# Optimization experiments

Hardware: AMD Instinct MI355X
Metric: run time of the kernel (lower is better)

Reference implementation:

```python
import jax, jax.numpy as jnp
import numpy as np
from jax import lax

B_, N_, DIM, HID, DST, NT, IR, DTR, HH, WW = 16, 4096, 192, 384, 16, 17, 128, 24, 64, 64


def _selective_scan(u, delta, A, Bs, Cs, D, delta_bias):
    # u, delta: (B, Din, L); A: (Din, N); Bs, Cs: (B, N, L); D, delta_bias: (Din,)
    delta = jax.nn.softplus(delta + delta_bias[None, :, None])
    dT = jnp.moveaxis(delta, 2, 0)   # (L, B, Din)
    uT = jnp.moveaxis(u, 2, 0)       # (L, B, Din)
    BT = jnp.moveaxis(Bs, 2, 0)      # (L, B, N)
    CT = jnp.moveaxis(Cs, 2, 0)      # (L, B, N)
    Bsz, Din, L = u.shape
    Nst = A.shape[1]
    h0 = jnp.zeros((Bsz, Din, Nst), u.dtype)

    def step(h, inp):
        d_l, u_l, b_l, c_l = inp
        da = jnp.exp(d_l[:, :, None] * A[None])              # (B, Din, N)
        h = da * h + (d_l * u_l)[:, :, None] * b_l[:, None, :]
        y = jnp.einsum('bdn,bn->bd', h, c_l)
        return h, y

    _, ys = lax.scan(step, h0, (dT, uT, BT, CT))
    y = jnp.moveaxis(ys, 0, 2)                               # (B, Din, L)
    return y + u * D[None, :, None]


def _assm_forward(x, token_weight, gumbel_noise, embB, route_w1, route_b1, route_w2,
                  route_b2, inproj_w, inproj_b, cpe_w, cpe_b, x_proj_w, dt_w, dt_b,
                  A_logs, Ds, norm_g, norm_b, outproj_w, outproj_b, H, W, gather_type):
    B, n, C = x.shape
    hidden = inproj_w.shape[0]
    dst = token_weight.shape[1]
    dtr = dt_w.shape[1]

    # routing + gumbel-softmax (hard, straight-through)
    full_emb = embB @ token_weight                           # (NT, d_state)
    hmid = jax.nn.gelu(x @ route_w1.T + route_b1)
    logits = jax.nn.log_softmax(hmid @ route_w2.T + route_b2, axis=-1)
    y_soft = jax.nn.softmax(logits + gumbel_noise, axis=-1)
    idx = jnp.argmax(y_soft, axis=-1)                        # (B, n)
    y_hard = jax.nn.one_hot(idx, logits.shape[-1], dtype=y_soft.dtype)
    cls_policy = y_hard + y_soft - lax.stop_gradient(y_soft)
    prompt = cls_policy @ full_emb                           # (B, n, d_state)

    det = lax.stop_gradient(idx)
    # (gather_type 3/5 keypoint-group remap omitted: gather_type == 1 here)
    sort_idx = jnp.argsort(det, axis=-1)                     # (B, n)
    inv_idx = jnp.argsort(sort_idx, axis=-1)                 # index_reverse

    # in_proj (1x1 conv == pointwise linear) then depthwise CPE gate
    xi = x @ inproj_w.T + inproj_b                           # (B, n, hidden)
    xg = xi.reshape(B, H, W, hidden).transpose(0, 3, 1, 2)   # NCHW
    cpe = lax.conv_general_dilated(xg, cpe_w, (1, 1), 'SAME',
                                   feature_group_count=hidden,
                                   dimension_numbers=('NCHW', 'OIHW', 'NCHW'))
    cpe = cpe + cpe_b[None, :, None, None]
    xg = xg * jax.nn.sigmoid(cpe)
    xflat = xg.reshape(B, hidden, n).transpose(0, 2, 1)      # (B, n, hidden)

    sem_x = jnp.take_along_axis(xflat, sort_idx[:, :, None], axis=1)

    # Selective_Scan core
    xs = sem_x.transpose(0, 2, 1)                            # (B, Din, L)
    x_dbl = jnp.einsum('bdl,cd->bcl', xs, x_proj_w)          # (B, dtr+2N, L)
    dts, Bs, Cs = jnp.split(x_dbl, [dtr, dtr + dst], axis=1)
    dts = jnp.einsum('brl,dr->bdl', dts, dt_w)
    if gather_type != 0:
        Cs = Cs + prompt.transpose(0, 2, 1)
    A = -jnp.exp(A_logs)
    y = _selective_scan(xs, dts, A, Bs, Cs, Ds, dt_b)        # (B, Din, L)
    y = y.transpose(0, 2, 1)                                 # (B, L, hidden)

    mu = jnp.mean(y, axis=-1, keepdims=True)
    var = jnp.mean(jnp.square(y - mu), axis=-1, keepdims=True)
    yn = (y - mu) / jnp.sqrt(var + 1e-5) * norm_g + norm_b
    out = yn @ outproj_w.T + outproj_b                       # (B, n, dim)
    out = jnp.take_along_axis(out, inv_idx[:, :, None], axis=1)
    return out


def setup_inputs() -> dict:
    key = jax.random.key(0)
    ks = jax.random.split(key, 16)

    def rn(k, sh, s=0.02):
        return jax.random.normal(k, sh, dtype=jnp.float32) * s

    u = jax.random.uniform(ks[0], (B_, N_, NT), jnp.float32, 1e-6, 1.0 - 1e-6)
    gumbel = -jnp.log(-jnp.log(u))

    # faithful dt bias init (inverse-softplus of log-uniform dt)
    rng = np.random.default_rng(0)
    dt = np.exp(rng.uniform(size=HID) * (np.log(0.1) - np.log(0.001)) + np.log(0.001))
    dt = np.clip(dt, 1e-4, None)
    inv_dt = dt + np.log(-np.expm1(-dt))

    A_logs = jnp.log(jnp.tile(jnp.arange(1, DST + 1, dtype=jnp.float32), (HID, 1)))

    return {
        'x': jax.random.normal(ks[1], (B_, N_, DIM), jnp.float32),
        'token_weight': rn(ks[2], (IR, DST), 0.1),
        'gumbel_noise': gumbel,
        'embB': jax.random.uniform(ks[3], (NT, IR), jnp.float32, -1.0 / NT, 1.0 / NT),
        'route_w1': rn(ks[4], (DIM // 3, DIM)),
        'route_b1': jnp.zeros((DIM // 3,), jnp.float32),
        'route_w2': rn(ks[5], (NT, DIM // 3)),
        'route_b2': jnp.zeros((NT,), jnp.float32),
        'inproj_w': rn(ks[6], (HID, DIM)),
        'inproj_b': jnp.zeros((HID,), jnp.float32),
        'cpe_w': rn(ks[7], (HID, 1, 3, 3), 0.1),
        'cpe_b': jnp.zeros((HID,), jnp.float32),
        'x_proj_w': rn(ks[8], (DTR + 2 * DST, HID)),
        'dt_w': jax.random.uniform(ks[9], (HID, DTR), jnp.float32, -DTR ** -0.5, DTR ** -0.5),
        'dt_b': jnp.asarray(inv_dt, jnp.float32),
        'A_logs': A_logs,
        'Ds': jnp.ones((HID,), jnp.float32),
        'norm_g': jnp.ones((HID,), jnp.float32),
        'norm_b': jnp.zeros((HID,), jnp.float32),
        'outproj_w': rn(ks[10], (DIM, HID)),
        'outproj_b': jnp.zeros((DIM,), jnp.float32),
        'H': HH,
        'W': WW,
        'gather_type': 1,
    }


def reference(x, token_weight, gumbel_noise, embB, route_w1, route_b1, route_w2,
              route_b2, inproj_w, inproj_b, cpe_w, cpe_b, x_proj_w, dt_w, dt_b,
              A_logs, Ds, norm_g, norm_b, outproj_w, outproj_b, H, W, gather_type):
    return _assm_forward(x, token_weight, gumbel_noise, embB, route_w1, route_b1,
                         route_w2, route_b2, inproj_w, inproj_b, cpe_w, cpe_b,
                         x_proj_w, dt_w, dt_b, A_logs, Ds, norm_g, norm_b,
                         outproj_w, outproj_b, H, W, gather_type)
```

## Files before the change

kernel.cpp:

```cpp
#include <hip/hip_runtime.h>
#include <math.h>

#define NB 16
#define NL 4096
#define ND 192
#define NH 384
#define NS 16
#define NTK 17
#define NIR 128
#define NR 24
#define NHH 64
#define NWW 64
#define NCHUNKS 64
#define CHUNKLEN 64
#define NTOK (NB*NL)

typedef __attribute__((ext_vector_type(8))) short short8;
typedef __attribute__((ext_vector_type(4))) float floatx4;

__device__ __forceinline__ float gelu_tanh(float x){
  return 0.5f*x*(1.0f + tanhf(0.7978845608028654f*(x + 0.044715f*x*x*x)));
}
__device__ __forceinline__ float softplus_f(float x){
  return (x > 20.0f) ? x : log1pf(expf(x));
}
__device__ __forceinline__ short f2bf(float f){
  unsigned u = __float_as_uint(f);
  unsigned r = (u + 0x7fffu + ((u >> 16) & 1u)) >> 16;
  return (short)r;
}

union Pack8 { uint4 v; short s[8]; };

__global__ void k_emb(const float* __restrict__ embB, const float* __restrict__ tw,
                      float* __restrict__ fe){
  for (int o = threadIdx.x; o < NTK*NS; o += 256){
    int t = o / NS, s = o % NS;
    float acc = 0.f;
    for (int i = 0; i < NIR; ++i) acc += embB[t*NIR+i]*tw[i*NS+s];
    fe[o] = acc;
  }
}

__global__ void k_cvtw(const float* __restrict__ inw, const float* __restrict__ ow,
                       const float* __restrict__ xpw, const float* __restrict__ dtw,
                       short* __restrict__ inwb, short* __restrict__ owb,
                       short* __restrict__ xpwb, short* __restrict__ dtwb){
  int i = blockIdx.x*256 + threadIdx.x;
  int stride = gridDim.x*256;
  for (int p = i; p < NH*ND; p += stride) inwb[p] = f2bf(inw[p]);
  for (int p = i; p < ND*NH; p += stride) owb[p] = f2bf(ow[p]);
  for (int p = i; p < 56*NH; p += stride) xpwb[p] = f2bf(xpw[p]);
  for (int p = i; p < NH*32; p += stride){
    int r = p >> 5, c = p & 31;
    dtwb[p] = (c < NR) ? f2bf(dtw[r*NR + c]) : (short)0;
  }
}

template<int EPI>
__global__ __launch_bounds__(256) void k_gemm(const float* __restrict__ A, int lda,
    const float* __restrict__ W, int ldw, const float* __restrict__ bias,
    float* __restrict__ C, int ldc, int N, int K){
  __shared__ float As[16][68];
  __shared__ float Ws[16][68];
  int tid = threadIdx.x;
  int m0 = blockIdx.x*64, n0 = blockIdx.y*64;
  int tx = tid & 15, ty = tid >> 4;
  int srow = tid >> 2, skseg = (tid & 3)*4;
  float acc[4][4] = {};
  for (int k0 = 0; k0 < K; k0 += 16){
    {
      const float* ap = A + (size_t)(m0+srow)*lda + k0 + skseg;
      float4 v = *(const float4*)ap;
      As[skseg+0][srow]=v.x; As[skseg+1][srow]=v.y;
      As[skseg+2][srow]=v.z; As[skseg+3][srow]=v.w;
    }
    {
      float4 v = {0.f,0.f,0.f,0.f};
      if (n0 + srow < N) v = *(const float4*)(W + (size_t)(n0+srow)*ldw + k0 + skseg);
      Ws[skseg+0][srow]=v.x; Ws[skseg+1][srow]=v.y;
      Ws[skseg+2][srow]=v.z; Ws[skseg+3][srow]=v.w;
    }
    __syncthreads();
    #pragma unroll
    for (int kk = 0; kk < 16; ++kk){
      float4 av = *(const float4*)&As[kk][ty*4];
      float4 wv = *(const float4*)&Ws[kk][tx*4];
      acc[0][0] += av.x*wv.x; acc[0][1] += av.x*wv.y;
      acc[0][2] += av.x*wv.z; acc[0][3] += av.x*wv.w;
      acc[1][0] += av.y*wv.x; acc[1][1] += av.y*wv.y;
      acc[1][2] += av.y*wv.z; acc[1][3] += av.y*wv.w;
      acc[2][0] += av.z*wv.x; acc[2][1] += av.z*wv.y;
      acc[2][2] += av.z*wv.z; acc[2][3] += av.z*wv.w;
      acc[3][0] += av.w*wv.x; acc[3][1] += av.w*wv.y;
      acc[3][2] += av.w*wv.z; acc[3][3] += av.w*wv.w;
    }
    __syncthreads();
  }
  #pragma unroll
  for (int i = 0; i < 4; ++i){
    int m = m0 + ty*4 + i;
    #pragma unroll
    for (int j = 0; j < 4; ++j){
      int n = n0 + tx*4 + j;
      if (n < N){
        float v = acc[i][j] + (bias ? bias[n] : 0.f);
        if (EPI==1) v = gelu_tanh(v);
        C[(size_t)m*ldc + n] = v;
      }
    }
  }
}

template<int EPI, int AF32, int LNA>
__global__ __launch_bounds__(256) void k_mfma(const void* __restrict__ Aptr, int lda,
    const short* __restrict__ Wbf, int ldw, const float* __restrict__ bias,
    float* __restrict__ C, int ldc, int N, int K, const int* __restrict__ remap,
    const float* __restrict__ lnm, const float* __restrict__ lnr,
    const float* __restrict__ lng, const float* __restrict__ lnb){
  __shared__ short As[128*40];
  __shared__ short Bs[64*40];
  int tid = threadIdx.x;
  int m0 = blockIdx.x*128, n0 = blockIdx.y*64;
  int w = tid >> 6, lane = tid & 63;
  int lq = lane >> 4, lr = lane & 15;
  floatx4 acc[2][4];
  #pragma unroll
  for (int i = 0; i < 2; ++i)
    #pragma unroll
    for (int j = 0; j < 4; ++j) acc[i][j] = (floatx4){0.f,0.f,0.f,0.f};
  int ar = tid >> 1, aq = (tid & 1)*2;
  int br = tid >> 2, bq = tid & 3;
  float mr = 0.f, rr = 0.f;
  if (LNA){ mr = lnm[m0+ar]; rr = lnr[m0+ar]; }
  for (int k0 = 0; k0 < K; k0 += 32){
    Pack8 sa0, sa1;
    if (AF32){
      const float* ap = (const float*)Aptr + (size_t)(m0+ar)*lda + k0 + aq*8;
      float f[16];
      float4 f0 = *(const float4*)(ap);
      float4 f1 = *(const float4*)(ap+4);
      float4 f2 = *(const float4*)(ap+8);
      float4 f3 = *(const float4*)(ap+12);
      f[0]=f0.x; f[1]=f0.y; f[2]=f0.z; f[3]=f0.w;
      f[4]=f1.x; f[5]=f1.y; f[6]=f1.z; f[7]=f1.w;
      f[8]=f2.x; f[9]=f2.y; f[10]=f2.z; f[11]=f2.w;
      f[12]=f3.x; f[13]=f3.y; f[14]=f3.z; f[15]=f3.w;
      if (LNA){
        const float* gp = lng + k0 + aq*8;
        const float* bp = lnb + k0 + aq*8;
        #pragma unroll
        for (int j = 0; j < 16; ++j) f[j] = (f[j]-mr)*rr*gp[j] + bp[j];
      }
      #pragma unroll
      for (int j = 0; j < 8; ++j){ sa0.s[j] = f2bf(f[j]); sa1.s[j] = f2bf(f[8+j]); }
    } else {
      const short* ap = (const short*)Aptr + (size_t)(m0+ar)*lda + k0 + aq*8;
      sa0.v = *(const uint4*)ap;
      sa1.v = *(const uint4*)(ap + 8);
    }
    uint4 bv = {0u,0u,0u,0u};
    if (n0 + br < N) bv = *(const uint4*)(Wbf + (size_t)(n0+br)*ldw + k0 + bq*8);
    __syncthreads();
    *(uint4*)&As[ar*40 + aq*8]     = sa0.v;
    *(uint4*)&As[ar*40 + aq*8 + 8] = sa1.v;
    *(uint4*)&Bs[br*40 + bq*8]     = bv;
    __syncthreads();
    short8 a0 = *(const short8*)&As[(w*32      + lr)*40 + lq*8];
    short8 a1 = *(const short8*)&As[(w*32 + 16 + lr)*40 + lq*8];
    short8 b0 = *(const short8*)&Bs[(     lr)*40 + lq*8];
    short8 b1 = *(const short8*)&Bs[(16 + lr)*40 + lq*8];
    short8 b2 = *(const short8*)&Bs[(32 + lr)*40 + lq*8];
    short8 b3 = *(const short8*)&Bs[(48 + lr)*40 + lq*8];
    acc[0][0] = __builtin_amdgcn_mfma_f32_16x16x32_bf16(a0, b0, acc[0][0], 0,0,0);
    acc[0][1] = __builtin_amdgcn_mfma_f32_16x16x32_bf16(a0, b1, acc[0][1], 0,0,0);
    acc[0][2] = __builtin_amdgcn_mfma_f32_16x16x32_bf16(a0, b2, acc[0][2], 0,0,0);
    acc[0][3] = __builtin_amdgcn_mfma_f32_16x16x32_bf16(a0, b3, acc[0][3], 0,0,0);
    acc[1][0] = __builtin_amdgcn_mfma_f32_16x16x32_bf16(a1, b0, acc[1][0], 0,0,0);
    acc[1][1] = __builtin_amdgcn_mfma_f32_16x16x32_bf16(a1, b1, acc[1][1], 0,0,0);
    acc[1][2] = __builtin_amdgcn_mfma_f32_16x16x32_bf16(a1, b2, acc[1][2], 0,0,0);
    acc[1][3] = __builtin_amdgcn_mfma_f32_16x16x32_bf16(a1, b3, acc[1][3], 0,0,0);
  }
  #pragma unroll
  for (int mt = 0; mt < 2; ++mt){
    #pragma unroll
    for (int r = 0; r < 4; ++r){
      int m = m0 + w*32 + mt*16 + lq*4 + r;
      int orow = (EPI==3) ? remap[m] : m;
      #pragma unroll
      for (int nt = 0; nt < 4; ++nt){
        int n = n0 + nt*16 + lr;
        if (n < N){
          float v = acc[mt][nt][r] + (bias ? bias[n] : 0.f);
          if (EPI==2) v = softplus_f(v);
          C[(size_t)orow*ldc + n] = v;
        }
      }
    }
  }
}

__global__ __launch_bounds__(256) void k_argmax(const float* __restrict__ hmid,
    const float* __restrict__ w2, const float* __restrict__ b2,
    const float* __restrict__ gumbel, int* __restrict__ idx){
  int g = blockIdx.x*256 + threadIdx.x;
  float hm[64];
  const float4* hp = (const float4*)(hmid + (size_t)g*64);
  #pragma unroll
  for (int i = 0; i < 16; ++i){
    float4 v = hp[i];
    hm[i*4+0]=v.x; hm[i*4+1]=v.y; hm[i*4+2]=v.z; hm[i*4+3]=v.w;
  }
  float best = -INFINITY; int bi = 0;
  for (int c = 0; c < NTK; ++c){
    float s = b2[c] + gumbel[(size_t)g*NTK + c];
    #pragma unroll
    for (int j = 0; j < 64; ++j) s += hm[j]*w2[c*64+j];
    if (s > best){ best = s; bi = c; }
  }
  idx[g] = bi;
}

__global__ __launch_bounds__(256) void k_sort(const int* __restrict__ idx,
    int* __restrict__ rmap, int* __restrict__ inv){
  int b = blockIdx.x, t = threadIdx.x;
  __shared__ int hist[NTK][256];
  __shared__ int tot[NTK];
  __shared__ int keybase[NTK];
  int keys[16];
  const int* ip = idx + b*NL + t*16;
  #pragma unroll
  for (int i = 0; i < 16; ++i) keys[i] = ip[i];
  #pragma unroll
  for (int k = 0; k < NTK; ++k){
    int c = 0;
    #pragma unroll
    for (int i = 0; i < 16; ++i) c += (keys[i]==k) ? 1 : 0;
    hist[k][t] = c;
  }
  __syncthreads();
  if (t < NTK){
    int run = 0;
    for (int j = 0; j < 256; ++j){ int v = hist[t][j]; hist[t][j] = run; run += v; }
    tot[t] = run;
  }
  __syncthreads();
  if (t == 0){
    int base = 0;
    for (int k = 0; k < NTK; ++k){ keybase[k] = base; base += tot[k]; }
  }
  __syncthreads();
  #pragma unroll
  for (int i = 0; i < 16; ++i){
    int k = keys[i];
    int cb = 0;
    #pragma unroll
    for (int j = 0; j < 16; ++j) cb += (j < i && keys[j]==k) ? 1 : 0;
    int pos = keybase[k] + hist[k][t] + cb;
    rmap[b*NL + pos] = b*NL + t*16 + i;
    inv[b*NL + t*16 + i] = pos;
  }
}

__global__ __launch_bounds__(384) void k_cpe(const float* __restrict__ xi,
    const float* __restrict__ cw, const float* __restrict__ cb,
    const int* __restrict__ inv, float* __restrict__ us){
  int bl = blockIdx.x;
  int cg = bl & 3;
  int xt = (bl>>2) & 7;
  int yt = (bl>>5) & 7;
  int b  = bl >> 8;
  __shared__ float tile[10*10*96];
  int tx = threadIdx.x;
  int ty = threadIdx.y;
  int c0 = cg*96;
  int ch = c0 + tx;
  for (int yy = 0; yy < 10; ++yy){
    int gy = yt*8 + yy - 1;
    for (int xx = ty; xx < 10; xx += 4){
      int gx = xt*8 + xx - 1;
      float v = 0.f;
      if (gy >= 0 && gy < NHH && gx >= 0 && gx < NWW)
        v = xi[((size_t)(b*NL + gy*NWW + gx))*NH + ch];
      tile[(yy*10 + xx)*96 + tx] = v;
    }
  }
  float wreg[9];
  #pragma unroll
  for (int j = 0; j < 9; ++j) wreg[j] = cw[ch*9 + j];
  float bias = cb[ch];
  __syncthreads();
  for (int yy = ty; yy < 8; yy += 4){
    #pragma unroll
    for (int xx = 0; xx < 8; ++xx){
      float acc = bias;
      #pragma unroll
      for (int dy = 0; dy < 3; ++dy)
        #pragma unroll
        for (int dx = 0; dx < 3; ++dx)
          acc += tile[((yy+dy)*10 + (xx+dx))*96 + tx] * wreg[dy*3+dx];
      float center = tile[((yy+1)*10 + (xx+1))*96 + tx];
      float gate = 1.f/(1.f + expf(-acc));
      int l = (yt*8+yy)*NWW + xt*8+xx;
      int pos = inv[b*NL + l];
      us[((size_t)(b*NL + pos))*NH + ch] = center*gate;
    }
  }
}

__global__ __launch_bounds__(256) void k_bc(const float* __restrict__ dbl,
    const int* __restrict__ idx, const float* __restrict__ fe,
    const int* __restrict__ gt, float* __restrict__ Bsb, float* __restrict__ Csb,
    short* __restrict__ dtsb){
  int g = blockIdx.x*256 + threadIdx.x;
  const float* dr = dbl + (size_t)g*56;
  int id = idx[g];
  int gather = gt[0];
  #pragma unroll
  for (int n = 0; n < NR; ++n) dtsb[(size_t)g*32 + n] = f2bf(dr[n]);
  #pragma unroll
  for (int n = NR; n < 32; ++n) dtsb[(size_t)g*32 + n] = 0;
  #pragma unroll
  for (int n = 0; n < NS; ++n){
    Bsb[(size_t)g*NS + n] = dr[24+n];
    float c = dr[40+n];
    if (gather != 0) c += fe[id*NS + n];
    Csb[(size_t)g*NS + n] = c;
  }
}

__device__ __forceinline__ void decay16(bool pw, float dlt, const float* An, float* a){
  if (pw){
    float r  = __expf(dlt*An[0]);
    float r2 = r*r;
    float r3 = r2*r;
    float r4 = r2*r2;
    float r8 = r4*r4;
    float r12 = r8*r4;
    a[0]=r;     a[1]=r2;     a[2]=r3;     a[3]=r4;
    a[4]=r4*r;  a[5]=r4*r2;  a[6]=r4*r3;  a[7]=r8;
    a[8]=r8*r;  a[9]=r8*r2;  a[10]=r8*r3; a[11]=r12;
    a[12]=r12*r; a[13]=r12*r2; a[14]=r12*r3; a[15]=r8*r8;
  } else {
    #pragma unroll
    for (int n = 0; n < NS; ++n) a[n] = __expf(dlt*An[n]);
  }
}
__device__ __forceinline__ bool pwcheck(const float* An){
  bool pw = true;
  #pragma unroll
  for (int n = 1; n < NS; ++n)
    pw = pw && (fabsf(An[n] - (n+1)*An[0]) <= 1e-4f*fabsf(An[n]));
  return pw;
}

__global__ __launch_bounds__(384) void k_scan1(const float* __restrict__ delta,
    const float* __restrict__ us, const float* __restrict__ Bsb,
    const float* __restrict__ A_logs, float* __restrict__ sds, float* __restrict__ Boff){
  int bc = blockIdx.x;
  int c = bc & (NCHUNKS-1);
  int b = bc >> 6;
  int d = threadIdx.x;
  int base = b*NL + c*CHUNKLEN;
  const float4* __restrict__ Bu = (const float4*)(Bsb + (size_t)base*NS);
  float An[NS];
  #pragma unroll
  for (int n = 0; n < NS; ++n) An[n] = -expf(A_logs[d*NS + n]);
  bool pw = pwcheck(An);
  float h[NS];
  #pragma unroll
  for (int n = 0; n < NS; ++n) h[n]=0.f;
  float sd = 0.f;
  const float* dp = delta + (size_t)base*NH + d;
  const float* up = us    + (size_t)base*NH + d;
  float pdlt[4], puv[4];
  #pragma unroll
  for (int j = 0; j < 4; ++j){ pdlt[j] = dp[(size_t)j*NH]; puv[j] = up[(size_t)j*NH]; }
  for (int s = 0; s < CHUNKLEN; s += 4){
    #pragma unroll
    for (int jj = 0; jj < 4; ++jj){
      float dltc = pdlt[jj], uvc = puv[jj];
      if (s + 4 < CHUNKLEN){
        pdlt[jj] = dp[(size_t)(s+4+jj)*NH];
        puv[jj]  = up[(size_t)(s+4+jj)*NH];
      }
      float4 bq0 = Bu[(s+jj)*4 + 0];
      float4 bq1 = Bu[(s+jj)*4 + 1];
      float4 bq2 = Bu[(s+jj)*4 + 2];
      float4 bq3 = Bu[(s+jj)*4 + 3];
      float du = dltc*uvc;
      sd += dltc;
      float a[NS];
      decay16(pw, dltc, An, a);
      h[0]  = a[0] *h[0]  + du*bq0.x;
      h[1]  = a[1] *h[1]  + du*bq0.y;
      h[2]  = a[2] *h[2]  + du*bq0.z;
      h[3]  = a[3] *h[3]  + du*bq0.w;
      h[4]  = a[4] *h[4]  + du*bq1.x;
      h[5]  = a[5] *h[5]  + du*bq1.y;
      h[6]  = a[6] *h[6]  + du*bq1.z;
      h[7]  = a[7] *h[7]  + du*bq1.w;
      h[8]  = a[8] *h[8]  + du*bq2.x;
      h[9]  = a[9] *h[9]  + du*bq2.y;
      h[10] = a[10]*h[10] + du*bq2.z;
      h[11] = a[11]*h[11] + du*bq2.w;
      h[12] = a[12]*h[12] + du*bq3.x;
      h[13] = a[13]*h[13] + du*bq3.y;
      h[14] = a[14]*h[14] + du*bq3.z;
      h[15] = a[15]*h[15] + du*bq3.w;
    }
  }
  sds[(size_t)bc*NH + d] = sd;
  size_t o = ((size_t)bc*NH + d)*NS;
  *(float4*)(Boff + o)      = make_float4(h[0], h[1], h[2], h[3]);
  *(float4*)(Boff + o + 4)  = make_float4(h[4], h[5], h[6], h[7]);
  *(float4*)(Boff + o + 8)  = make_float4(h[8], h[9], h[10],h[11]);
  *(float4*)(Boff + o + 12) = make_float4(h[12],h[13],h[14],h[15]);
}

__global__ __launch_bounds__(256) void k_scan2(const float* __restrict__ A_logs,
    const float* __restrict__ sds, float* __restrict__ Boff){
  int i = blockIdx.x*256 + threadIdx.x;
  int dn = i % (NH*NS);
  int b = i / (NH*NS);
  float An = -expf(A_logs[dn]);
  int d = dn >> 4;
  const float* sp = sds + (size_t)(b*NCHUNKS)*NH + d;
  float* bp = Boff + (size_t)(b*NCHUNKS)*(NH*NS) + dn;
  float sdp[4], bop[4];
  #pragma unroll
  for (int j = 0; j < 4; ++j){
    sdp[j] = sp[(size_t)j*NH];
    bop[j] = bp[(size_t)j*(NH*NS)];
  }
  float h = 0.f;
  for (int c = 0; c < NCHUNKS; c += 4){
    #pragma unroll
    for (int jj = 0; jj < 4; ++jj){
      float sdc = sdp[jj], boc = bop[jj];
      if (c + 4 < NCHUNKS){
        sdp[jj] = sp[(size_t)(c+4+jj)*NH];
        bop[jj] = bp[(size_t)(c+4+jj)*(NH*NS)];
      }
      float a = __expf(sdc*An);
      bp[(size_t)(c+jj)*(NH*NS)] = h;
      h = a*h + boc;
    }
  }
}

__global__ __launch_bounds__(384) void k_scan3(const float* __restrict__ delta,
    const float* __restrict__ Bsb, const float* __restrict__ Csb,
    const float* __restrict__ A_logs, const float* __restrict__ Ds,
    const float* __restrict__ hinit, float* __restrict__ us){
  int bc = blockIdx.x;
  int c = bc & (NCHUNKS-1);
  int b = bc >> 6;
  int d = threadIdx.x;
  int base = b*NL + c*CHUNKLEN;
  const float4* __restrict__ Bu = (const float4*)(Bsb + (size_t)base*NS);
  const float4* __restrict__ Cu = (const float4*)(Csb + (size_t)base*NS);
  float An[NS];
  #pragma unroll
  for (int n = 0; n < NS; ++n) An[n] = -expf(A_logs[d*NS + n]);
  bool pw = pwcheck(An);
  float h[NS];
  size_t ho = ((size_t)bc*NH + d)*NS;
  {
    float4 h0 = *(const float4*)(hinit + ho);
    float4 h1 = *(const float4*)(hinit + ho + 4);
    float4 h2 = *(const float4*)(hinit + ho + 8);
    float4 h3 = *(const float4*)(hinit + ho + 12);
    h[0]=h0.x; h[1]=h0.y; h[2]=h0.z; h[3]=h0.w;
    h[4]=h1.x; h[5]=h1.y; h[6]=h1.z; h[7]=h1.w;
    h[8]=h2.x; h[9]=h2.y; h[10]=h2.z; h[11]=h2.w;
    h[12]=h3.x; h[13]=h3.y; h[14]=h3.z; h[15]=h3.w;
  }
  float Dd = Ds[d];
  const float* dp = delta + (size_t)base*NH + d;
  float* up = us + (size_t)base*NH + d;
  float pdlt[4], puv[4];
  #pragma unroll
  for (int j = 0; j < 4; ++j){ pdlt[j] = dp[(size_t)j*NH]; puv[j] = up[(size_t)j*NH]; }
  for (int s = 0; s < CHUNKLEN; s += 4){
    #pragma unroll
    for (int jj = 0; jj < 4; ++jj){
      float dltc = pdlt[jj], uvc = puv[jj];
      if (s + 4 < CHUNKLEN){
        pdlt[jj] = dp[(size_t)(s+4+jj)*NH];
        puv[jj]  = up[(size_t)(s+4+jj)*NH];
      }
      float4 bq0 = Bu[(s+jj)*4 + 0];
      float4 bq1 = Bu[(s+jj)*4 + 1];
      float4 bq2 = Bu[(s+jj)*4 + 2];
      float4 bq3 = Bu[(s+jj)*4 + 3];
      float4 cq0 = Cu[(s+jj)*4 + 0];
      float4 cq1 = Cu[(s+jj)*4 + 1];
      float4 cq2 = Cu[(s+jj)*4 + 2];
      float4 cq3 = Cu[(s+jj)*4 + 3];
      float du = dltc*uvc;
      float a[NS];
      decay16(pw, dltc, An, a);
      h[0]  = a[0] *h[0]  + du*bq0.x;
      h[1]  = a[1] *h[1]  + du*bq0.y;
      h[2]  = a[2] *h[2]  + du*bq0.z;
      h[3]  = a[3] *h[3]  + du*bq0.w;
      h[4]  = a[4] *h[4]  + du*bq1.x;
      h[5]  = a[5] *h[5]  + du*bq1.y;
      h[6]  = a[6] *h[6]  + du*bq1.z;
      h[7]  = a[7] *h[7]  + du*bq1.w;
      h[8]  = a[8] *h[8]  + du*bq2.x;
      h[9]  = a[9] *h[9]  + du*bq2.y;
      h[10] = a[10]*h[10] + du*bq2.z;
      h[11] = a[11]*h[11] + du*bq2.w;
      h[12] = a[12]*h[12] + du*bq3.x;
      h[13] = a[13]*h[13] + du*bq3.y;
      h[14] = a[14]*h[14] + du*bq3.z;
      h[15] = a[15]*h[15] + du*bq3.w;
      float ya = h[0]*cq0.x + h[1]*cq0.y;
      ya += h[2]*cq0.z;  ya += h[3]*cq0.w;
      float yb = h[4]*cq1.x + h[5]*cq1.y;
      yb += h[6]*cq1.z;  yb += h[7]*cq1.w;
      float yc = h[8]*cq2.x + h[9]*cq2.y;
      yc += h[10]*cq2.z; yc += h[11]*cq2.w;
      float yd = h[12]*cq3.x + h[13]*cq3.y;
      yd += h[14]*cq3.z; yd += h[15]*cq3.w;
      float y = (ya+yb)+(yc+yd);
      up[(size_t)(s+jj)*NH] = y + uvc*Dd;
    }
  }
}

__global__ __launch_bounds__(256) void k_lnstat(const float* __restrict__ y,
    float* __restrict__ mean, float* __restrict__ rstd){
  int g = blockIdx.x*4 + (threadIdx.x >> 6);
  int lane = threadIdx.x & 63;
  size_t ro = (size_t)g*NH;
  float v[6];
  #pragma unroll
  for (int i = 0; i < 6; ++i) v[i] = y[ro + i*64 + lane];
  float s = 0.f;
  #pragma unroll
  for (int i = 0; i < 6; ++i) s += v[i];
  #pragma unroll
  for (int off = 32; off > 0; off >>= 1) s += __shfl_xor(s, off);
  float mu = s * (1.f/NH);
  float vs = 0.f;
  #pragma unroll
  for (int i = 0; i < 6; ++i){ float d = v[i]-mu; vs += d*d; }
  #pragma unroll
  for (int off = 32; off > 0; off >>= 1) vs += __shfl_xor(vs, off);
  float rs = rsqrtf(vs*(1.f/NH) + 1e-5f);
  if (lane == 0){ mean[g] = mu; rstd[g] = rs; }
}

extern "C" void kernel_launch(void* const* d_in, const int* in_sizes, int n_in,
                              void* d_out, int out_size, void* d_ws, size_t ws_size,
                              hipStream_t stream){
  const float* x      = (const float*)d_in[0];
  const float* tw     = (const float*)d_in[1];
  const float* gumbel = (const float*)d_in[2];
  const float* embB   = (const float*)d_in[3];
  const float* rw1    = (const float*)d_in[4];
  const float* rb1    = (const float*)d_in[5];
  const float* rw2    = (const float*)d_in[6];
  const float* rb2    = (const float*)d_in[7];
  const float* inw    = (const float*)d_in[8];
  const float* inb    = (const float*)d_in[9];
  const float* cw     = (const float*)d_in[10];
  const float* cb     = (const float*)d_in[11];
  const float* xpw    = (const float*)d_in[12];
  const float* dtw    = (const float*)d_in[13];
  const float* dtb    = (const float*)d_in[14];
  const float* A_logs = (const float*)d_in[15];
  const float* Ds     = (const float*)d_in[16];
  const float* ng     = (const float*)d_in[17];
  const float* nbv    = (const float*)d_in[18];
  const float* ow     = (const float*)d_in[19];
  const float* ob     = (const float*)d_in[20];
  const int*   gt     = (const int*)d_in[23];
  float* out = (float*)d_out;

  float* ws = (float*)d_ws;
  size_t o = 0;
  float* fe   = ws + o; o += 512;
  int* idx    = (int*)(ws + o); o += NTOK;
  int* rmap   = (int*)(ws + o); o += NTOK;
  int* inv    = (int*)(ws + o); o += NTOK;
  float* hmid = ws + o; o += (size_t)NTOK*64;
  float* xi   = ws + o; o += (size_t)NTOK*NH;
  float* us   = ws + o; o += (size_t)NTOK*NH;
  float* Bsb  = ws + o; o += (size_t)NTOK*NS;
  float* Csb  = ws + o; o += (size_t)NTOK*NS;
  float* sds  = ws + o; o += (size_t)NB*NCHUNKS*NH;
  float* Bof  = ws + o; o += (size_t)NB*NCHUNKS*NH*NS;
  short* inwb = (short*)(ws + o); o += (NH*ND)/2;
  short* owb  = (short*)(ws + o); o += (ND*NH)/2;
  short* xpwb = (short*)(ws + o); o += (56*NH)/2 + 32;
  short* dtwb = (short*)(ws + o); o += (NH*32)/2;
  float* dbl = hmid;
  float* delta = xi;
  short* dtsb = (short*)Bof;
  float* lnmean = (float*)idx;
  float* lnrstd = (float*)inv;

  k_emb<<<1,256,0,stream>>>(embB, tw, fe);
  k_cvtw<<<64,256,0,stream>>>(inw, ow, xpw, dtw, inwb, owb, xpwb, dtwb);
  k_gemm<1><<<dim3(NTOK/64,1),256,0,stream>>>(x, ND, rw1, ND, rb1, hmid, 64, 64, ND);
  k_argmax<<<NTOK/256,256,0,stream>>>(hmid, rw2, rb2, gumbel, idx);
  k_sort<<<NB,256,0,stream>>>(idx, rmap, inv);
  k_mfma<0,1,0><<<dim3(NTOK/128,6),256,0,stream>>>(x, ND, inwb, ND, inb, xi, NH, NH, ND,
      nullptr, nullptr, nullptr, nullptr, nullptr);
  k_cpe<<<NB*64*4,dim3(96,4),0,stream>>>(xi, cw, cb, inv, us);
  k_mfma<0,1,0><<<dim3(NTOK/128,1),256,0,stream>>>(us, NH, xpwb, NH, nullptr, dbl, 56, 56, NH,
      nullptr, nullptr, nullptr, nullptr, nullptr);
  k_bc<<<NTOK/256,256,0,stream>>>(dbl, idx, fe, gt, Bsb, Csb, dtsb);
  k_mfma<2,0,0><<<dim3(NTOK/128,6),256,0,stream>>>(dtsb, 32, dtwb, 32, dtb, delta, NH, NH, 32,
      nullptr, nullptr, nullptr, nullptr, nullptr);
  k_scan1<<<NB*NCHUNKS,384,0,stream>>>(delta, us, Bsb, A_logs, sds, Bof);
  k_scan2<<<(NB*NH*NS)/256,256,0,stream>>>(A_logs, sds, Bof);
  k_scan3<<<NB*NCHUNKS,384,0,stream>>>(delta, Bsb, Csb, A_logs, Ds, Bof, us);
  k_lnstat<<<NTOK/4,256,0,stream>>>(us, lnmean, lnrstd);
  k_mfma<3,1,1><<<dim3(NTOK/128,3),256,0,stream>>>(us, NH, owb, NH, ob, out, ND, ND, NH,
      rmap, lnmean, lnrstd, ng, nbv);
}
```

Before: 800.1 us.

## Stage scan B/C in shared memory, lengthen chunks, fold embedding into weight-convert kernel

The chunked selective scan now uses 32 chunks of 128 steps instead of 64 of 64, halving the chunk-carry work in scan2. The per-chunk B and C vectors are loaded once into LDS, so the 384 threads read them from shared memory instead of each issuing broadcast global loads. The tiny embedding matmul kernel is merged into the weight-conversion kernel to save a launch. Longer chunks also halve the block count of scan1 and scan3 (512 blocks), which can reduce occupancy and lengthen each thread's serial dependency chain.

```diff
diff --git a/kernel.cpp b/kernel.cpp
--- a/kernel.cpp
+++ b/kernel.cpp
@@ -11,8 +11,8 @@
 #define NR 24
 #define NHH 64
 #define NWW 64
-#define NCHUNKS 64
-#define CHUNKLEN 64
+#define NCHUNKS 32
+#define CHUNKLEN 128
 #define NTOK (NB*NL)
 
 typedef __attribute__((ext_vector_type(8))) short short8;
@@ -32,20 +32,12 @@
 
 union Pack8 { uint4 v; short s[8]; };
 
-__global__ void k_emb(const float* __restrict__ embB, const float* __restrict__ tw,
-                      float* __restrict__ fe){
-  for (int o = threadIdx.x; o < NTK*NS; o += 256){
-    int t = o / NS, s = o % NS;
-    float acc = 0.f;
-    for (int i = 0; i < NIR; ++i) acc += embB[t*NIR+i]*tw[i*NS+s];
-    fe[o] = acc;
-  }
-}
-
 __global__ void k_cvtw(const float* __restrict__ inw, const float* __restrict__ ow,
                        const float* __restrict__ xpw, const float* __restrict__ dtw,
                        short* __restrict__ inwb, short* __restrict__ owb,
-                       short* __restrict__ xpwb, short* __restrict__ dtwb){
+                       short* __restrict__ xpwb, short* __restrict__ dtwb,
+                       const float* __restrict__ embB, const float* __restrict__ tw,
+                       float* __restrict__ fe){
   int i = blockIdx.x*256 + threadIdx.x;
   int stride = gridDim.x*256;
   for (int p = i; p < NH*ND; p += stride) inwb[p] = f2bf(inw[p]);
@@ -54,6 +46,14 @@
   for (int p = i; p < NH*32; p += stride){
     int r = p >> 5, c = p & 31;
     dtwb[p] = (c < NR) ? f2bf(dtw[r*NR + c]) : (short)0;
+  }
+  if (blockIdx.x == 0){
+    for (int o = threadIdx.x; o < NTK*NS; o += 256){
+      int t = o / NS, s = o % NS;
+      float acc = 0.f;
+      for (int k = 0; k < NIR; ++k) acc += embB[t*NIR+k]*tw[k*NS+s];
+      fe[o] = acc;
+    }
   }
 }
 
@@ -359,10 +359,14 @@
     const float* __restrict__ A_logs, float* __restrict__ sds, float* __restrict__ Boff){
   int bc = blockIdx.x;
   int c = bc & (NCHUNKS-1);
-  int b = bc >> 6;
+  int b = bc >> 5;
   int d = threadIdx.x;
+  __shared__ float4 Bsh[CHUNKLEN*4];
   int base = b*NL + c*CHUNKLEN;
-  const float4* __restrict__ Bu = (const float4*)(Bsb + (size_t)base*NS);
+  {
+    const float4* Bg = (const float4*)(Bsb + (size_t)base*NS);
+    for (int p = d; p < CHUNKLEN*4; p += 384) Bsh[p] = Bg[p];
+  }
   float An[NS];
   #pragma unroll
   for (int n = 0; n < NS; ++n) An[n] = -expf(A_logs[d*NS + n]);
@@ -371,6 +375,7 @@
   #pragma unroll
   for (int n = 0; n < NS; ++n) h[n]=0.f;
   float sd = 0.f;
+  __syncthreads();
   const float* dp = delta + (size_t)base*NH + d;
   const float* up = us    + (size_t)base*NH + d;
   float pdlt[4], puv[4];
@@ -384,30 +389,15 @@
         pdlt[jj] = dp[(size_t)(s+4+jj)*NH];
         puv[jj]  = up[(size_t)(s+4+jj)*NH];
       }
-      float4 bq0 = Bu[(s+jj)*4 + 0];
-      float4 bq1 = Bu[(s+jj)*4 + 1];
-      float4 bq2 = Bu[(s+jj)*4 + 2];
-      float4 bq3 = Bu[(s+jj)*4 + 3];
       float du = dltc*uvc;
       sd += dltc;
       float a[NS];
       decay16(pw, dltc, An, a);
-      h[0]  = a[0] *h[0]  + du*bq0.x;
-      h[1]  = a[1] *h[1]  + du*bq0.y;
-      h[2]  = a[2] *h[2]  + du*bq0.z;
-      h[3]  = a[3] *h[3]  + du*bq0.w;
-      h[4]  = a[4] *h[4]  + du*bq1.x;
-      h[5]  = a[5] *h[5]  + du*bq1.y;
-      h[6]  = a[6] *h[6]  + du*bq1.z;
-      h[7]  = a[7] *h[7]  + du*bq1.w;
-      h[8]  = a[8] *h[8]  + du*bq2.x;
-      h[9]  = a[9] *h[9]  + du*bq2.y;
-      h[10] = a[10]*h[10] + du*bq2.z;
-      h[11] = a[11]*h[11] + du*bq2.w;
-      h[12] = a[12]*h[12] + du*bq3.x;
-      h[13] = a[13]*h[13] + du*bq3.y;
-      h[14] = a[14]*h[14] + du*bq3.z;
-      h[15] = a[15]*h[15] + du*bq3.w;
+      float bb[NS];
+      #pragma unroll
+      for (int q = 0; q < 4; ++q) *(float4*)&bb[4*q] = Bsh[(s+jj)*4 + q];
+      #pragma unroll
+      for (int n = 0; n < NS; ++n) h[n] = a[n]*h[n] + du*bb[n];
     }
   }
   sds[(size_t)bc*NH + d] = sd;
@@ -455,11 +445,19 @@
     const float* __restrict__ hinit, float* __restrict__ us){
   int bc = blockIdx.x;
   int c = bc & (NCHUNKS-1);
-  int b = bc >> 6;
+  int b = bc >> 5;
   int d = threadIdx.x;
+  __shared__ float4 Bsh[CHUNKLEN*4];
+  __shared__ float4 Csh[CHUNKLEN*4];
   int base = b*NL + c*CHUNKLEN;
-  const float4* __restrict__ Bu = (const float4*)(Bsb + (size_t)base*NS);
-  const float4* __restrict__ Cu = (const float4*)(Csb + (size_t)base*NS);
+  {
+    const float4* Bg = (const float4*)(Bsb + (size_t)base*NS);
+    const float4* Cg = (const float4*)(Csb + (size_t)base*NS);
+    for (int p = d; p < CHUNKLEN*4; p += 384){
+      Bsh[p] = Bg[p];
+      Csh[p] = Cg[p];
+    }
+  }
   float An[NS];
   #pragma unroll
   for (int n = 0; n < NS; ++n) An[n] = -expf(A_logs[d*NS + n]);
@@ -477,6 +475,7 @@
     h[12]=h3.x; h[13]=h3.y; h[14]=h3.z; h[15]=h3.w;
   }
   float Dd = Ds[d];
+  __syncthreads();
   const float* dp = delta + (size_t)base*NH + d;
   float* up = us + (size_t)base*NH + d;
   float pdlt[4], puv[4];
@@ -490,41 +489,25 @@
         pdlt[jj] = dp[(size_t)(s+4+jj)*NH];
         puv[jj]  = up[(size_t)(s+4+jj)*NH];
       }
-      float4 bq0 = Bu[(s+jj)*4 + 0];
-      float4 bq1 = Bu[(s+jj)*4 + 1];
-      float4 bq2 = Bu[(s+jj)*4 + 2];
-      float4 bq3 = Bu[(s+jj)*4 + 3];
-      float4 cq0 = Cu[(s+jj)*4 + 0];
-      float4 cq1 = Cu[(s+jj)*4 + 1];
-      float4 cq2 = Cu[(s+jj)*4 + 2];
-      float4 cq3 = Cu[(s+jj)*4 + 3];
       float du = dltc*uvc;
       float a[NS];
       decay16(pw, dltc, An, a);
-      h[0]  = a[0] *h[0]  + du*bq0.x;
-      h[1]  = a[1] *h[1]  + du*bq0.y;
-      h[2]  = a[2] *h[2]  + du*bq0.z;
-      h[3]  = a[3] *h[3]  + du*bq0.w;
-      h[4]  = a[4] *h[4]  + du*bq1.x;
-      h[5]  = a[5] *h[5]  + du*bq1.y;
-      h[6]  = a[6] *h[6]  + du*bq1.z;
-      h[7]  = a[7] *h[7]  + du*bq1.w;
-      h[8]  = a[8] *h[8]  + du*bq2.x;
-      h[9]  = a[9] *h[9]  + du*bq2.y;
-      h[10] = a[10]*h[10] + du*bq2.z;
-      h[11] = a[11]*h[11] + du*bq2.w;
-      h[12] = a[12]*h[12] + du*bq3.x;
-      h[13] = a[13]*h[13] + du*bq3.y;
-      h[14] = a[14]*h[14] + du*bq3.z;
-      h[15] = a[15]*h[15] + du*bq3.w;
-      float ya = h[0]*cq0.x + h[1]*cq0.y;
-      ya += h[2]*cq0.z;  ya += h[3]*cq0.w;
-      float yb = h[4]*cq1.x + h[5]*cq1.y;
-      yb += h[6]*cq1.z;  yb += h[7]*cq1.w;
-      float yc = h[8]*cq2.x + h[9]*cq2.y;
-      yc += h[10]*cq2.z; yc += h[11]*cq2.w;
-      float yd = h[12]*cq3.x + h[13]*cq3.y;
-      yd += h[14]*cq3.z; yd += h[15]*cq3.w;
+      float bb[NS], cc[NS];
+      #pragma unroll
+      for (int q = 0; q < 4; ++q){
+        *(float4*)&bb[4*q] = Bsh[(s+jj)*4 + q];
+        *(float4*)&cc[4*q] = Csh[(s+jj)*4 + q];
+      }
+      #pragma unroll
+      for (int n = 0; n < NS; ++n) h[n] = a[n]*h[n] + du*bb[n];
+      float ya = 0.f, yb = 0.f, yc = 0.f, yd = 0.f;
+      #pragma unroll
+      for (int q = 0; q < 4; ++q){
+        ya += h[q]*cc[q];
+        yb += h[4+q]*cc[4+q];
+        yc += h[8+q]*cc[8+q];
+        yd += h[12+q]*cc[12+q];
+      }
       float y = (ya+yb)+(yc+yd);
       up[(size_t)(s+jj)*NH] = y + uvc*Dd;
     }
@@ -604,8 +587,7 @@
   float* lnmean = (float*)idx;
   float* lnrstd = (float*)inv;
 
-  k_emb<<<1,256,0,stream>>>(embB, tw, fe);
-  k_cvtw<<<64,256,0,stream>>>(inw, ow, xpw, dtw, inwb, owb, xpwb, dtwb);
+  k_cvtw<<<64,256,0,stream>>>(inw, ow, xpw, dtw, inwb, owb, xpwb, dtwb, embB, tw, fe);
   k_gemm<1><<<dim3(NTOK/64,1),256,0,stream>>>(x, ND, rw1, ND, rb1, hmid, 64, 64, ND);
   k_argmax<<<NTOK/256,256,0,stream>>>(hmid, rw2, rb2, gumbel, idx);
   k_sort<<<NB,256,0,stream>>>(idx, rmap, inv);
```

New measurement: 810.1 us. About the same (+1.3%).
